# Kernel optimization log

Hardware: AMD Instinct MI355X
Metric: run time of the kernel (lower is better)

## Reference

```python
import math
import jax, jax.numpy as jnp
import numpy as np

N = 50000
C = 128      # in_channels == out_channels
H = 8        # nhead
D = C // H   # head_dim = 16
E = 800000


def _layernorm(x, g, b, eps=1e-5):
    mu = jnp.mean(x, axis=-1, keepdims=True)
    var = jnp.var(x, axis=-1, keepdims=True)
    return (x - mu) * jax.lax.rsqrt(var + eps) * g + b


def setup_inputs() -> dict:
    key = jax.random.key(0)
    ks = jax.random.split(key, 12)
    s = 1.0 / math.sqrt(C)          # ~xavier scale
    s4 = 1.0 / math.sqrt(4 * C)
    return {
        "x": jax.random.normal(ks[0], (N, C), dtype=jnp.float32),
        "edge_index": jax.random.randint(ks[1], (2, E), 0, N, dtype=jnp.int64),
        "Wq": jax.random.normal(ks[2], (C, C), dtype=jnp.float32) * s,
        "Wk": jax.random.normal(ks[3], (C, C), dtype=jnp.float32) * s,
        "Wv": jax.random.normal(ks[4], (C, C), dtype=jnp.float32) * s,
        "Wo": jax.random.normal(ks[5], (C, C), dtype=jnp.float32) * s,
        "bo": jnp.zeros((C,), dtype=jnp.float32),
        "Wf1": jax.random.normal(ks[6], (C, 4 * C), dtype=jnp.float32) * s,
        "bf1": jnp.zeros((4 * C,), dtype=jnp.float32),
        "Wf2": jax.random.normal(ks[7], (4 * C, C), dtype=jnp.float32) * s4,
        "bf2": jnp.zeros((C,), dtype=jnp.float32),
        "g1": jnp.ones((C,), dtype=jnp.float32),
        "b1": jnp.zeros((C,), dtype=jnp.float32),
        "g2": jnp.ones((C,), dtype=jnp.float32),
        "b2": jnp.zeros((C,), dtype=jnp.float32),
    }


def reference(x, edge_index, Wq, Wk, Wv, Wo, bo, Wf1, bf1, Wf2, bf2, g1, b1, g2, b2):
    n = x.shape[0]
    loops = jnp.arange(n, dtype=edge_index.dtype)
    row = jnp.concatenate([edge_index[0], loops])  # source nodes
    col = jnp.concatenate([edge_index[1], loops])  # destination nodes

    q = (x @ Wq).reshape(n, H, D)
    k = (x @ Wk).reshape(n, H, D)
    v = (x @ Wv).reshape(n, H, D)

    # edge-level attention scores [E+N, H]
    scores = jnp.einsum('ehd,ehd->eh', q[row], k[col]) / math.sqrt(D)
    smax = jax.ops.segment_max(scores, col, num_segments=n)  # every node has a self-loop
    exp = jnp.exp(scores - smax[col])
    ssum = jax.ops.segment_sum(exp, col, num_segments=n)
    alpha = exp / (ssum[col] + 1e-8)

    out = jax.ops.segment_sum(v[row] * alpha[..., None], col, num_segments=n)
    attn = out.reshape(n, C) @ Wo + bo

    residual = x  # input_proj is Identity (in_channels == out_channels)
    x1 = _layernorm(residual + attn, g1, b1)
    ffn = jax.nn.gelu(x1 @ Wf1 + bf1, approximate=False) @ Wf2 + bf2
    return _layernorm(x1 + ffn, g2, b2)
```

## Files before the change

kernel.cpp:

```cpp
#include <hip/hip_runtime.h>
#include <cmath>


typedef short bf16x8 __attribute__((ext_vector_type(8)));
typedef float f32x4 __attribute__((ext_vector_type(4)));
typedef unsigned int uint_as1 __attribute__((address_space(1)));
typedef unsigned int uint_as3 __attribute__((address_space(3)));

__device__ inline unsigned short f2bf(float f) {
    unsigned int u = __float_as_uint(f);
    u += 0x7fffu + ((u >> 16) & 1u);
    return (unsigned short)(u >> 16);
}
__device__ inline float bflo(unsigned int w) { return __uint_as_float(w << 16); }
__device__ inline float bfhi(unsigned int w) { return __uint_as_float(w & 0xffff0000u); }

__device__ inline void gload16(const unsigned short* g, unsigned short* l) {
    __builtin_amdgcn_global_load_lds((const uint_as1*)g, (uint_as3*)l, 16, 0, 0);
}

__device__ inline float gelu_f(float x) {
    float ax = fabsf(x) * 0.70710678118f;
    float t = __builtin_amdgcn_rcpf(fmaf(0.3275911f, ax, 1.0f));
    float p = fmaf(1.061405429f, t, -1.453152027f);
    p = fmaf(p, t, 1.421413741f);
    p = fmaf(p, t, -0.284496736f);
    p = fmaf(p, t, 0.254829592f);
    p = p * t;
    float e = __expf(-ax * ax);
    float pe = p * e;
    float w = (x >= 0.f) ? (2.0f - pe) : pe;
    return 0.5f * x * w;
}


__device__ __forceinline__ void stage_panel(unsigned short* Bs,
                                            const unsigned short* base,
                                            int strideK) {
    int tid = threadIdx.x;
    int srow = tid >> 4, cc = tid & 15;
    int gc = (cc & ~7) | ((cc & 7) ^ (srow & 7));
    const unsigned short* src = base + (size_t)srow * strideK + gc * 8;
    unsigned short* dst = Bs + srow * 128 + cc * 8;
#pragma unroll
    for (int j = 0; j < 8; ++j)
        gload16(src + (size_t)j * 16 * strideK, dst + j * 16 * 128);
}

__device__ __forceinline__ void loadA_k(bf16x8 (&af)[4][4],
                                        const unsigned short* A, int M, int K,
                                        int m0, int ko, int wr, int l16, int quad) {
#pragma unroll
    for (int ti = 0; ti < 4; ++ti) {
        int row = m0 + wr * 64 + ti * 16 + l16;
        if (row > M - 1) row = M - 1;
        const unsigned short* ar = A + (size_t)row * K + ko + quad * 8;
#pragma unroll
        for (int j = 0; j < 4; ++j) af[ti][j] = *(const bf16x8*)(ar + j * 32);
    }
}

__device__ __forceinline__ void mm16(f32x4 (&acc)[4][4], const bf16x8 (&af)[4][4],
                                     const unsigned short* Bs,
                                     int wc, int quad, int l16) {
#pragma unroll
    for (int ks = 0; ks < 4; ++ks) {
        bf16x8 bfr[4];
#pragma unroll
        for (int tj = 0; tj < 4; ++tj) {
            int nr = wc * 64 + tj * 16 + l16;
            int cidx = ks * 4 + quad;
            int slot = (cidx & ~7) | ((cidx & 7) ^ (nr & 7));
            bfr[tj] = *(const bf16x8*)&Bs[nr * 128 + slot * 8];
        }
#pragma unroll
        for (int ti = 0; ti < 4; ++ti)
#pragma unroll
            for (int tj = 0; tj < 4; ++tj)
                acc[ti][tj] = __builtin_amdgcn_mfma_f32_16x16x32_bf16(
                    af[ti][ks], bfr[tj], acc[ti][tj], 0, 0, 0);
    }
}


__global__ __launch_bounds__(256) void k_init(
    const float* __restrict__ x, unsigned short* __restrict__ xb,
    const float* __restrict__ Wq, const float* __restrict__ Wk,
    const float* __restrict__ Wv, const float* __restrict__ Wo,
    const float* __restrict__ Wf1, const float* __restrict__ Wf2,
    unsigned short* __restrict__ Wqkvt, unsigned short* __restrict__ Wot,
    unsigned short* __restrict__ Wf1t, unsigned short* __restrict__ Wf2t,
    int* __restrict__ cursor, int4* __restrict__ csrz,
    int N, int nCsr4, int nCast) {
    int bid = blockIdx.x;
    int t = threadIdx.x;

    int NBc = (N + 255) >> 8;
    if (bid < NBc) {
        int i = bid * 256 + t;
        if (i < N) cursor[i] = 0;
        return;
    }
    bid -= NBc;
    int NBz = (nCsr4 + 255) >> 8;
    if (bid < NBz) {
        int i = bid * 256 + t;
        if (i < nCsr4) csrz[i] = make_int4(0, 0, 0, 0);
        return;
    }
    bid -= NBz;
    if (bid < nCast) {
        int i = bid * 256 + t;
        if (i < N * 32) {
            float4 v = ((const float4*)x)[i];
            ushort4 o;
            o.x = f2bf(v.x); o.y = f2bf(v.y); o.z = f2bf(v.z); o.w = f2bf(v.w);
            ((ushort4*)xb)[i] = o;
        }
        return;
    }
    bid -= nCast;
    int z, idx;
    if (bid < 256) { z = bid >> 6; idx = (bid & 63) * 256 + t; }
    else           { z = 4 + ((bid - 256) >> 8); idx = ((bid - 256) & 255) * 256 + t; }

    const float* in; unsigned short* out; int K, Co;
    switch (z) {
        case 0: in = Wq;  out = Wqkvt; K = 128; Co = 128; break;
        case 1: in = Wk;  out = Wqkvt; K = 128; Co = 128; break;
        case 2: in = Wv;  out = Wqkvt; K = 128; Co = 128; break;
        case 3: in = Wo;  out = Wot;   K = 128; Co = 128; break;
        case 4: in = Wf1; out = Wf1t;  K = 128; Co = 512; break;
        default: in = Wf2; out = Wf2t; K = 512; Co = 128; break;
    }
    if (idx >= K * Co) return;
    int k = idx / Co, c = idx % Co;
    int row;
    switch (z) {
        case 0: row = ((c >> 1) << 2) | (c & 1); break;
        case 1: row = 256 + c; break;
        case 2: row = (((c >> 1) << 2) | (c & 1)) + 2; break;
        default: row = c; break;
    }
    out[(size_t)row * K + k] = f2bf(in[idx]);
}


__global__ void k_fill(const int* __restrict__ ei, int* __restrict__ cursor,
                       unsigned short* __restrict__ csr, int E, int N) {
    int e = blockIdx.x * 256 + threadIdx.x;
    if (e >= E + N) return;
    int row, col;
    if (e < E) { row = ei[e]; col = ei[E + e]; }
    else       { row = col = e - E; }
    int pos = atomicAdd(&cursor[col], 1);
    csr[(size_t)col * 64 + pos] = (unsigned short)row;
}


template <int EPI, int MT>
__global__ __launch_bounds__(256) void k_gemmM(
    const unsigned short* __restrict__ A, const unsigned short* __restrict__ Bt,
    const float* __restrict__ bias, const float* __restrict__ resid,
    const float* __restrict__ g, const float* __restrict__ b,
    float* __restrict__ outf, unsigned short* __restrict__ outb,
    int M, int Cout, int NZ) {
    __shared__ unsigned short Bs[128 * 128];
    __shared__ float pS[2][128], pQ[2][128];

    int tid = threadIdx.x;
    int wid = tid >> 6, lane = tid & 63;
    int quad = lane >> 4, l16 = lane & 15;
    int wr = wid >> 1, wc = wid & 1;
    int bid = blockIdx.x;
    int zi = bid % NZ;
    int ci = bid / NZ;
    int n0 = zi * 128;

    stage_panel(Bs, Bt + (size_t)n0 * 128, 128);
    __syncthreads();
#pragma unroll
    for (int mt = 0; mt < MT; ++mt) {
        int m0 = (ci * MT + mt) * 128;
        if (m0 >= M) continue;

        bf16x8 af[4][4];
        loadA_k(af, A, M, 128, m0, 0, wr, l16, quad);

        f32x4 acc[4][4];
#pragma unroll
        for (int i = 0; i < 4; ++i)
#pragma unroll
            for (int j = 0; j < 4; ++j) acc[i][j] = {0.f, 0.f, 0.f, 0.f};
        mm16(acc, af, Bs, wc, quad, l16);

        if constexpr (EPI != 2) {
            float bi[4];
            if constexpr (EPI == 1) {
#pragma unroll
                for (int tj = 0; tj < 4; ++tj)
                    bi[tj] = bias[n0 + wc * 64 + tj * 16 + l16];
            }
#pragma unroll
            for (int ti = 0; ti < 4; ++ti)
#pragma unroll
                for (int tj = 0; tj < 4; ++tj) {
                    int col = n0 + wc * 64 + tj * 16 + l16;
#pragma unroll
                    for (int r = 0; r < 4; ++r) {
                        int row = m0 + wr * 64 + ti * 16 + quad * 4 + r;
                        if (row >= M) continue;
                        float v = acc[ti][tj][r];
                        if constexpr (EPI == 1) v = gelu_f(v + bi[tj]);
                        outb[(size_t)row * Cout + col] = f2bf(v);
                    }
                }
        } else {
            float bi[4], gv[4], bv[4];
#pragma unroll
            for (int tj = 0; tj < 4; ++tj) {
                int col = wc * 64 + tj * 16 + l16;
                bi[tj] = bias[col]; gv[tj] = g[col]; bv[tj] = b[col];
            }
#pragma unroll
            for (int ti = 0; ti < 4; ++ti)
#pragma unroll
                for (int tj = 0; tj < 4; ++tj) {
                    int col = wc * 64 + tj * 16 + l16;
#pragma unroll
                    for (int r = 0; r < 4; ++r) {
                        int row = m0 + wr * 64 + ti * 16 + quad * 4 + r;
                        float rv = (row < M) ? resid[(size_t)row * 128 + col] : 0.f;
                        acc[ti][tj][r] += bi[tj] + rv;
                    }
                }
#pragma unroll
            for (int ti = 0; ti < 4; ++ti)
#pragma unroll
                for (int r = 0; r < 4; ++r) {
                    float s = acc[ti][0][r] + acc[ti][1][r] + acc[ti][2][r] + acc[ti][3][r];
                    float q = acc[ti][0][r] * acc[ti][0][r] + acc[ti][1][r] * acc[ti][1][r]
                            + acc[ti][2][r] * acc[ti][2][r] + acc[ti][3][r] * acc[ti][3][r];
                    s += __shfl_xor(s, 1); q += __shfl_xor(q, 1);
                    s += __shfl_xor(s, 2); q += __shfl_xor(q, 2);
                    s += __shfl_xor(s, 4); q += __shfl_xor(q, 4);
                    s += __shfl_xor(s, 8); q += __shfl_xor(q, 8);
                    if (l16 == 0) {
                        int lr = wr * 64 + ti * 16 + quad * 4 + r;
                        pS[wc][lr] = s; pQ[wc][lr] = q;
                    }
                }
            __syncthreads();
            if (tid < 128) {
                float s = pS[0][tid] + pS[1][tid];
                float q = pQ[0][tid] + pQ[1][tid];
                float mean = s * 0.0078125f;
                float var = q * 0.0078125f - mean * mean;
                pS[0][tid] = mean;
                pQ[0][tid] = rsqrtf(var + 1e-5f);
            }
            __syncthreads();
#pragma unroll
            for (int ti = 0; ti < 4; ++ti)
#pragma unroll
                for (int r = 0; r < 4; ++r) {
                    int lr = wr * 64 + ti * 16 + quad * 4 + r;
                    int row = m0 + lr;
                    if (row >= M) continue;
                    float mean = pS[0][lr], rs = pQ[0][lr];
#pragma unroll
                    for (int tj = 0; tj < 4; ++tj) {
                        int col = wc * 64 + tj * 16 + l16;
                        float y = (acc[ti][tj][r] - mean) * rs * gv[tj] + bv[tj];
                        if (outf) outf[(size_t)row * 128 + col] = y;
                        if (outb) outb[(size_t)row * 128 + col] = f2bf(y);
                    }
                }
        }
    }
}


template <int KT>
__global__ __launch_bounds__(256) void k_gemmK(
    const unsigned short* __restrict__ A, const unsigned short* __restrict__ Bt,
    const float* __restrict__ bias, const float* __restrict__ resid,
    const float* __restrict__ g, const float* __restrict__ b,
    float* __restrict__ outf, int M) {
    constexpr int K = KT * 128;
    __shared__ unsigned short smem[128 * 128];
    __shared__ float pS[2][128], pQ[2][128];

    int tid = threadIdx.x;
    int wid = tid >> 6, lane = tid & 63;
    int quad = lane >> 4, l16 = lane & 15;
    int wr = wid >> 1, wc = wid & 1;
    int m0 = blockIdx.x * 128;

    f32x4 acc[4][4];
#pragma unroll
    for (int i = 0; i < 4; ++i)
#pragma unroll
        for (int j = 0; j < 4; ++j) acc[i][j] = {0.f, 0.f, 0.f, 0.f};

#pragma unroll
    for (int kt = 0; kt < KT; ++kt) {
        bf16x8 af[4][4];
        loadA_k(af, A, M, K, m0, kt * 128, wr, l16, quad);
        stage_panel(smem, Bt + kt * 128, K);
        __syncthreads();
        mm16(acc, af, smem, wc, quad, l16);
        __syncthreads();
    }

    float bi[4], gv[4], bv[4];
#pragma unroll
    for (int tj = 0; tj < 4; ++tj) {
        int col = wc * 64 + tj * 16 + l16;
        bi[tj] = bias[col]; gv[tj] = g[col]; bv[tj] = b[col];
    }
#pragma unroll
    for (int ti = 0; ti < 4; ++ti)
#pragma unroll
        for (int tj = 0; tj < 4; ++tj) {
            int col = wc * 64 + tj * 16 + l16;
#pragma unroll
            for (int r = 0; r < 4; ++r) {
                int row = m0 + wr * 64 + ti * 16 + quad * 4 + r;
                float rv = (row < M) ? resid[(size_t)row * 128 + col] : 0.f;
                acc[ti][tj][r] += bi[tj] + rv;
            }
        }
#pragma unroll
    for (int ti = 0; ti < 4; ++ti)
#pragma unroll
        for (int r = 0; r < 4; ++r) {
            float s = acc[ti][0][r] + acc[ti][1][r] + acc[ti][2][r] + acc[ti][3][r];
            float q = acc[ti][0][r] * acc[ti][0][r] + acc[ti][1][r] * acc[ti][1][r]
                    + acc[ti][2][r] * acc[ti][2][r] + acc[ti][3][r] * acc[ti][3][r];
            s += __shfl_xor(s, 1); q += __shfl_xor(q, 1);
            s += __shfl_xor(s, 2); q += __shfl_xor(q, 2);
            s += __shfl_xor(s, 4); q += __shfl_xor(q, 4);
            s += __shfl_xor(s, 8); q += __shfl_xor(q, 8);
            if (l16 == 0) {
                int lr = wr * 64 + ti * 16 + quad * 4 + r;
                pS[wc][lr] = s; pQ[wc][lr] = q;
            }
        }
    __syncthreads();
    if (tid < 128) {
        float s = pS[0][tid] + pS[1][tid];
        float q = pQ[0][tid] + pQ[1][tid];
        float mean = s * 0.0078125f;
        float var = q * 0.0078125f - mean * mean;
        pS[0][tid] = mean;
        pQ[0][tid] = rsqrtf(var + 1e-5f);
    }
    __syncthreads();
#pragma unroll
    for (int ti = 0; ti < 4; ++ti)
#pragma unroll
        for (int r = 0; r < 4; ++r) {
            int lr = wr * 64 + ti * 16 + quad * 4 + r;
            int row = m0 + lr;
            if (row >= M) continue;
            float mean = pS[0][lr], rs = pQ[0][lr];
#pragma unroll
            for (int tj = 0; tj < 4; ++tj) {
                int col = wc * 64 + tj * 16 + l16;
                outf[(size_t)row * 128 + col] =
                    (acc[ti][tj][r] - mean) * rs * gv[tj] + bv[tj];
            }
        }
}


__global__ __launch_bounds__(256) void k_attn(
    const unsigned int* __restrict__ qkv, const int* __restrict__ counts,
    const unsigned short* __restrict__ csr, unsigned int* __restrict__ ob,
    int N) {
    int j = blockIdx.x * 4 + (threadIdx.x >> 6);
    if (j >= N) return;
    int l = threadIdx.x & 63;
    int lk = l & 31;
    int half = l >> 5;
    const uint4* qv4 = (const uint4*)qkv;

    uint2 kw = *(const uint2*)(qkv + (size_t)j * 192 + 128 + lk * 2);
    const float S = 0.36067376022224085f;
    float k0 = bflo(kw.x) * S, k1 = bfhi(kw.x) * S;
    float k2 = bflo(kw.y) * S, k3 = bfhi(kw.y) * S;

    int cnt = counts[j];
    int nb = (cnt + 3) >> 2;
    const unsigned short* cp = csr + (size_t)j * 64;

    int ra0 = cp[half],     rb0 = cp[2 + half];
    int ra1 = cp[4 + half], rb1 = cp[6 + half];
    uint4 gA = qv4[(unsigned)ra0 * 48u + lk];
    uint4 gB = qv4[(unsigned)rb0 * 48u + lk];

    float lsum = 0.f, a0 = 0.f, a1 = 0.f, a2 = 0.f, a3 = 0.f;
    for (int bi = 0; bi < nb; ++bi) {
        int ra2 = cp[(bi + 2) * 4 + half];
        int rb2 = cp[(bi + 2) * 4 + 2 + half];
        uint4 nA = qv4[(unsigned)ra1 * 48u + lk];
        uint4 nB = qv4[(unsigned)rb1 * 48u + lk];

        int rem = cnt - bi * 4;
        {
            float s = fmaf(bflo(gA.x), k0,
                      fmaf(bfhi(gA.x), k1,
                      fmaf(bflo(gA.z), k2, bfhi(gA.z) * k3)));
            s += __shfl_xor(s, 1);
            s += __shfl_xor(s, 2);
            float e = exp2f(s);
            e = (half < rem) ? e : 0.f;
            lsum += e;
            a0 = fmaf(e, bflo(gA.y), a0); a1 = fmaf(e, bfhi(gA.y), a1);
            a2 = fmaf(e, bflo(gA.w), a2); a3 = fmaf(e, bfhi(gA.w), a3);
        }
        {
            float s = fmaf(bflo(gB.x), k0,
                      fmaf(bfhi(gB.x), k1,
                      fmaf(bflo(gB.z), k2, bfhi(gB.z) * k3)));
            s += __shfl_xor(s, 1);
            s += __shfl_xor(s, 2);
            float e = exp2f(s);
            e = (2 + half < rem) ? e : 0.f;
            lsum += e;
            a0 = fmaf(e, bflo(gB.y), a0); a1 = fmaf(e, bfhi(gB.y), a1);
            a2 = fmaf(e, bflo(gB.w), a2); a3 = fmaf(e, bfhi(gB.w), a3);
        }
        gA = nA; gB = nB; ra1 = ra2; rb1 = rb2;
    }

    lsum += __shfl_xor(lsum, 32);
    a0 += __shfl_xor(a0, 32); a1 += __shfl_xor(a1, 32);
    a2 += __shfl_xor(a2, 32); a3 += __shfl_xor(a3, 32);

    if (half == 0) {
        float inv = 1.f / (lsum + 1e-8f);
        uint2 o;
        o.x = ((unsigned int)f2bf(a1 * inv) << 16) | (unsigned int)f2bf(a0 * inv);
        o.y = ((unsigned int)f2bf(a3 * inv) << 16) | (unsigned int)f2bf(a2 * inv);
        *(uint2*)(ob + (size_t)j * 64 + lk * 2) = o;
    }
}


extern "C" void kernel_launch(void* const* d_in, const int* in_sizes, int n_in,
                              void* d_out, int out_size, void* d_ws, size_t ws_size,
                              hipStream_t stream) {
    const float* x   = (const float*)d_in[0];
    const int* ei    = (const int*)d_in[1];
    const float* Wq  = (const float*)d_in[2];
    const float* Wk  = (const float*)d_in[3];
    const float* Wv  = (const float*)d_in[4];
    const float* Wo  = (const float*)d_in[5];
    const float* bo  = (const float*)d_in[6];
    const float* Wf1 = (const float*)d_in[7];
    const float* bf1 = (const float*)d_in[8];
    const float* Wf2 = (const float*)d_in[9];
    const float* bf2 = (const float*)d_in[10];
    const float* g1  = (const float*)d_in[11];
    const float* b1  = (const float*)d_in[12];
    const float* g2  = (const float*)d_in[13];
    const float* b2  = (const float*)d_in[14];

    int N = in_sizes[0] / 128;
    int E = in_sizes[1] / 2;
    int N2 = ((N + 127) / 128) * 128;
    int NE = E + N;

    char* p = (char*)d_ws;
    auto alloc = [&](size_t bytes) -> char* {
        char* r = p;
        p += (bytes + 255) & ~(size_t)255;
        return r;
    };
    unsigned short* qkv = (unsigned short*)alloc((size_t)N2 * 512 * 2);
    unsigned short* ob  = qkv + (size_t)N2 * 384;
    unsigned short* hb  = qkv;
    unsigned short* x1b = (unsigned short*)alloc((size_t)N2 * 128 * 2);
    unsigned short* xb  = x1b;
    float* x1f          = (float*)alloc((size_t)N2 * 128 * 4);
    unsigned short* Wqkvt = (unsigned short*)alloc(384 * 128 * 2);
    unsigned short* Wot   = (unsigned short*)alloc(128 * 128 * 2);
    unsigned short* Wf1t  = (unsigned short*)alloc(512 * 128 * 2);
    unsigned short* Wf2t  = (unsigned short*)alloc(128 * 512 * 2);
    int* cursor = (int*)alloc((size_t)N * 4);
    unsigned short* csr = (unsigned short*)alloc(((size_t)N * 64 + 256) * 2);

    int nCsr4 = N * 8 + 32;
    int nCast = (N * 32 + 255) / 256;
    int nInit = ((N + 255) / 256) + ((nCsr4 + 255) / 256) + nCast + 768;
    int M128 = (N + 127) / 128;
    int MC2  = (M128 + 1) / 2;

    k_init<<<nInit, 256, 0, stream>>>(x, xb, Wq, Wk, Wv, Wo, Wf1, Wf2,
                                      Wqkvt, Wot, Wf1t, Wf2t,
                                      cursor, (int4*)csr, N, nCsr4, nCast);
    k_fill<<<(NE + 255) / 256, 256, 0, stream>>>(ei, cursor, csr, E, N);

    k_gemmM<0, 2><<<3 * MC2, 256, 0, stream>>>(
        xb, Wqkvt, nullptr, nullptr, nullptr, nullptr, nullptr, qkv,
        N, 384, 3);

    k_attn<<<(N + 3) / 4, 256, 0, stream>>>((const unsigned int*)qkv, cursor,
                                            csr, (unsigned int*)ob, N);

    k_gemmM<2, 1><<<M128, 256, 0, stream>>>(
        ob, Wot, bo, x, g1, b1, x1f, x1b, N, 128, 1);

    k_gemmM<1, 2><<<4 * MC2, 256, 0, stream>>>(
        x1b, Wf1t, bf1, nullptr, nullptr, nullptr, nullptr, hb, N, 512, 4);

    k_gemmK<4><<<M128, 256, 0, stream>>>(
        hb, Wf2t, bf2, x1f, g2, b2, (float*)d_out, N);
}
```

Measured before the change: 349.9 us.

## Give each wave full-width 16-row strips so LayerNorm stays in registers

```diff
diff --git a/kernel.cpp b/kernel.cpp
--- a/kernel.cpp
+++ b/kernel.cpp
@@ -47,6 +47,16 @@
         gload16(src + (size_t)j * 16 * strideK, dst + j * 16 * 128);
 }
 
+__device__ __forceinline__ void loadA16(bf16x8 (&af)[4],
+                                        const unsigned short* A, int M, int K,
+                                        int base, int ko, int l16, int quad) {
+    int row = base + l16;
+    if (row > M - 1) row = M - 1;
+    const unsigned short* ar = A + (size_t)row * K + ko + quad * 8;
+#pragma unroll
+    for (int j = 0; j < 4; ++j) af[j] = *(const bf16x8*)(ar + j * 32);
+}
+
 __device__ __forceinline__ void loadA_k(bf16x8 (&af)[4][4],
                                         const unsigned short* A, int M, int K,
                                         int m0, int ko, int wr, int l16, int quad) {
@@ -158,126 +168,124 @@
 }
 
 
-template <int EPI, int MT>
-__global__ __launch_bounds__(256) void k_gemmM(
+template <int EPI>
+__global__ __launch_bounds__(256) void k_gemmP(
     const unsigned short* __restrict__ A, const unsigned short* __restrict__ Bt,
     const float* __restrict__ bias, const float* __restrict__ resid,
     const float* __restrict__ g, const float* __restrict__ b,
     float* __restrict__ outf, unsigned short* __restrict__ outb,
     int M, int Cout, int NZ) {
     __shared__ unsigned short Bs[128 * 128];
-    __shared__ float pS[2][128], pQ[2][128];
 
     int tid = threadIdx.x;
-    int wid = tid >> 6, lane = tid & 63;
+    int w = tid >> 6, lane = tid & 63;
     int quad = lane >> 4, l16 = lane & 15;
-    int wr = wid >> 1, wc = wid & 1;
-    int bid = blockIdx.x;
-    int zi = bid % NZ;
-    int ci = bid / NZ;
+    int zi = blockIdx.x % NZ;
+    int ci = blockIdx.x / NZ;
     int n0 = zi * 128;
 
     stage_panel(Bs, Bt + (size_t)n0 * 128, 128);
+
+    float bi[8], gv[8], bv[8];
+    if constexpr (EPI >= 1) {
+#pragma unroll
+        for (int tj = 0; tj < 8; ++tj) bi[tj] = bias[n0 * (EPI == 1) + tj * 16 + l16];
+    }
+    if constexpr (EPI == 2) {
+#pragma unroll
+        for (int tj = 0; tj < 8; ++tj) {
+            gv[tj] = g[tj * 16 + l16];
+            bv[tj] = b[tj * 16 + l16];
+        }
+    }
+
+    int base0 = ci * 128 + w * 16;
+    int base1 = base0 + 64;
+    bf16x8 afA[4], afB[4];
+    loadA16(afA, A, M, 128, base0, 0, l16, quad);
+    loadA16(afB, A, M, 128, base1, 0, l16, quad);
     __syncthreads();
-#pragma unroll
-    for (int mt = 0; mt < MT; ++mt) {
-        int m0 = (ci * MT + mt) * 128;
-        if (m0 >= M) continue;
-
-        bf16x8 af[4][4];
-        loadA_k(af, A, M, 128, m0, 0, wr, l16, quad);
-
-        f32x4 acc[4][4];
-#pragma unroll
-        for (int i = 0; i < 4; ++i)
-#pragma unroll
-            for (int j = 0; j < 4; ++j) acc[i][j] = {0.f, 0.f, 0.f, 0.f};
-        mm16(acc, af, Bs, wc, quad, l16);
-
-        if constexpr (EPI != 2) {
-            float bi[4];
-            if constexpr (EPI == 1) {
-#pragma unroll
-                for (int tj = 0; tj < 4; ++tj)
-                    bi[tj] = bias[n0 + wc * 64 + tj * 16 + l16];
-            }
-#pragma unroll
-            for (int ti = 0; ti < 4; ++ti)
-#pragma unroll
-                for (int tj = 0; tj < 4; ++tj) {
-                    int col = n0 + wc * 64 + tj * 16 + l16;
-#pragma unroll
-                    for (int r = 0; r < 4; ++r) {
-                        int row = m0 + wr * 64 + ti * 16 + quad * 4 + r;
-                        if (row >= M) continue;
-                        float v = acc[ti][tj][r];
-                        if constexpr (EPI == 1) v = gelu_f(v + bi[tj]);
-                        outb[(size_t)row * Cout + col] = f2bf(v);
+
+    auto tile = [&](const bf16x8 (&af)[4], int base) {
+        f32x4 acc[8];
+#pragma unroll
+        for (int tj = 0; tj < 8; ++tj) acc[tj] = {0.f, 0.f, 0.f, 0.f};
+#pragma unroll
+        for (int ks = 0; ks < 4; ++ks) {
+            int cidx = ks * 4 + quad;
+#pragma unroll
+            for (int tj = 0; tj < 8; ++tj) {
+                int nr = tj * 16 + l16;
+                int slot = (cidx & ~7) | ((cidx & 7) ^ (nr & 7));
+                bf16x8 bfr = *(const bf16x8*)&Bs[nr * 128 + slot * 8];
+                acc[tj] = __builtin_amdgcn_mfma_f32_16x16x32_bf16(
+                    af[ks], bfr, acc[tj], 0, 0, 0);
+            }
+        }
+        if constexpr (EPI == 0) {
+#pragma unroll
+            for (int tj = 0; tj < 8; ++tj) {
+                int col = n0 + tj * 16 + l16;
+#pragma unroll
+                for (int r = 0; r < 4; ++r) {
+                    int row = base + quad * 4 + r;
+                    if (row < M) outb[(size_t)row * Cout + col] = f2bf(acc[tj][r]);
+                }
+            }
+        } else if constexpr (EPI == 1) {
+#pragma unroll
+            for (int tj = 0; tj < 8; ++tj) {
+                int col = n0 + tj * 16 + l16;
+#pragma unroll
+                for (int r = 0; r < 4; ++r) {
+                    int row = base + quad * 4 + r;
+                    if (row < M)
+                        outb[(size_t)row * Cout + col] = f2bf(gelu_f(acc[tj][r] + bi[tj]));
+                }
+            }
+        } else {
+#pragma unroll
+            for (int tj = 0; tj < 8; ++tj) {
+                int col = tj * 16 + l16;
+#pragma unroll
+                for (int r = 0; r < 4; ++r) {
+                    int row = base + quad * 4 + r;
+                    float rv = (row < M) ? resid[(size_t)row * 128 + col] : 0.f;
+                    acc[tj][r] += bi[tj] + rv;
+                }
+            }
+#pragma unroll
+            for (int r = 0; r < 4; ++r) {
+                float s = 0.f, q = 0.f;
+#pragma unroll
+                for (int tj = 0; tj < 8; ++tj) {
+                    s += acc[tj][r];
+                    q += acc[tj][r] * acc[tj][r];
+                }
+                s += __shfl_xor(s, 1); q += __shfl_xor(q, 1);
+                s += __shfl_xor(s, 2); q += __shfl_xor(q, 2);
+                s += __shfl_xor(s, 4); q += __shfl_xor(q, 4);
+                s += __shfl_xor(s, 8); q += __shfl_xor(q, 8);
+                float mean = s * 0.0078125f;
+                float var = q * 0.0078125f - mean * mean;
+                float rs = rsqrtf(var + 1e-5f);
+                int row = base + quad * 4 + r;
+                bool ok = row < M;
+#pragma unroll
+                for (int tj = 0; tj < 8; ++tj) {
+                    int col = tj * 16 + l16;
+                    float y = (acc[tj][r] - mean) * rs * gv[tj] + bv[tj];
+                    if (ok) {
+                        outf[(size_t)row * 128 + col] = y;
+                        outb[(size_t)row * 128 + col] = f2bf(y);
                     }
                 }
-        } else {
-            float bi[4], gv[4], bv[4];
-#pragma unroll
-            for (int tj = 0; tj < 4; ++tj) {
-                int col = wc * 64 + tj * 16 + l16;
-                bi[tj] = bias[col]; gv[tj] = g[col]; bv[tj] = b[col];
-            }
-#pragma unroll
-            for (int ti = 0; ti < 4; ++ti)
-#pragma unroll
-                for (int tj = 0; tj < 4; ++tj) {
-                    int col = wc * 64 + tj * 16 + l16;
-#pragma unroll
-                    for (int r = 0; r < 4; ++r) {
-                        int row = m0 + wr * 64 + ti * 16 + quad * 4 + r;
-                        float rv = (row < M) ? resid[(size_t)row * 128 + col] : 0.f;
-                        acc[ti][tj][r] += bi[tj] + rv;
-                    }
-                }
-#pragma unroll
-            for (int ti = 0; ti < 4; ++ti)
-#pragma unroll
-                for (int r = 0; r < 4; ++r) {
-                    float s = acc[ti][0][r] + acc[ti][1][r] + acc[ti][2][r] + acc[ti][3][r];
-                    float q = acc[ti][0][r] * acc[ti][0][r] + acc[ti][1][r] * acc[ti][1][r]
-                            + acc[ti][2][r] * acc[ti][2][r] + acc[ti][3][r] * acc[ti][3][r];
-                    s += __shfl_xor(s, 1); q += __shfl_xor(q, 1);
-                    s += __shfl_xor(s, 2); q += __shfl_xor(q, 2);
-                    s += __shfl_xor(s, 4); q += __shfl_xor(q, 4);
-                    s += __shfl_xor(s, 8); q += __shfl_xor(q, 8);
-                    if (l16 == 0) {
-                        int lr = wr * 64 + ti * 16 + quad * 4 + r;
-                        pS[wc][lr] = s; pQ[wc][lr] = q;
-                    }
-                }
-            __syncthreads();
-            if (tid < 128) {
-                float s = pS[0][tid] + pS[1][tid];
-                float q = pQ[0][tid] + pQ[1][tid];
-                float mean = s * 0.0078125f;
-                float var = q * 0.0078125f - mean * mean;
-                pS[0][tid] = mean;
-                pQ[0][tid] = rsqrtf(var + 1e-5f);
-            }
-            __syncthreads();
-#pragma unroll
-            for (int ti = 0; ti < 4; ++ti)
-#pragma unroll
-                for (int r = 0; r < 4; ++r) {
-                    int lr = wr * 64 + ti * 16 + quad * 4 + r;
-                    int row = m0 + lr;
-                    if (row >= M) continue;
-                    float mean = pS[0][lr], rs = pQ[0][lr];
-#pragma unroll
-                    for (int tj = 0; tj < 4; ++tj) {
-                        int col = wc * 64 + tj * 16 + l16;
-                        float y = (acc[ti][tj][r] - mean) * rs * gv[tj] + bv[tj];
-                        if (outf) outf[(size_t)row * 128 + col] = y;
-                        if (outb) outb[(size_t)row * 128 + col] = f2bf(y);
-                    }
-                }
-        }
-    }
+            }
+        }
+    };
+
+    tile(afA, base0);
+    tile(afB, base1);
 }
 
 
@@ -496,24 +504,23 @@
     int nCast = (N * 32 + 255) / 256;
     int nInit = ((N + 255) / 256) + ((nCsr4 + 255) / 256) + nCast + 768;
     int M128 = (N + 127) / 128;
-    int MC2  = (M128 + 1) / 2;
 
     k_init<<<nInit, 256, 0, stream>>>(x, xb, Wq, Wk, Wv, Wo, Wf1, Wf2,
                                       Wqkvt, Wot, Wf1t, Wf2t,
                                       cursor, (int4*)csr, N, nCsr4, nCast);
     k_fill<<<(NE + 255) / 256, 256, 0, stream>>>(ei, cursor, csr, E, N);
 
-    k_gemmM<0, 2><<<3 * MC2, 256, 0, stream>>>(
+    k_gemmP<0><<<3 * M128, 256, 0, stream>>>(
         xb, Wqkvt, nullptr, nullptr, nullptr, nullptr, nullptr, qkv,
         N, 384, 3);
 
     k_attn<<<(N + 3) / 4, 256, 0, stream>>>((const unsigned int*)qkv, cursor,
                                             csr, (unsigned int*)ob, N);
 
-    k_gemmM<2, 1><<<M128, 256, 0, stream>>>(
+    k_gemmP<2><<<M128, 256, 0, stream>>>(
         ob, Wot, bo, x, g1, b1, x1f, x1b, N, 128, 1);
 
-    k_gemmM<1, 2><<<4 * MC2, 256, 0, stream>>>(
+    k_gemmP<1><<<4 * M128, 256, 0, stream>>>(
         x1b, Wf1t, bf1, nullptr, nullptr, nullptr, nullptr, hb, N, 512, 4);
 
     k_gemmK<4><<<M128, 256, 0, stream>>>(
```

Result: faster. 319.8 us (-8.6%).
